# Optimization experiments

Measured on AMD Instinct MI355X. Metric: run time of the kernel, lower is better.

## Reference

```python
import jax, jax.numpy as jnp
import numpy as np

DIM = 1024
NUM_HEADS = 16
HEAD_DIM = DIM // NUM_HEADS


def apply_rotary_embed(x, thetas):
    # x: (..., seq, d), thetas: (seq, d) broadcast over leading dims
    x1, x2 = jnp.split(x, 2, axis=-1)
    x_rot = jnp.concatenate([-x2, x1], axis=-1)
    return x * jnp.cos(thetas) + x_rot * jnp.sin(thetas)


def setup_inputs() -> dict:
    key = jax.random.key(0)
    ks = jax.random.split(key, 8)
    B, Nx, Nc = 4, 1024, 2048
    x = jax.random.normal(ks[0], (B, Nx, DIM), dtype=jnp.float32)
    c = jax.random.normal(ks[1], (B, Nc, DIM), dtype=jnp.float32)
    x_pos_embed = jax.random.normal(ks[2], (Nx, HEAD_DIM), dtype=jnp.float32)
    c_pos_embed = jax.random.normal(ks[3], (Nc, HEAD_DIM), dtype=jnp.float32)
    s = 1.0 / np.sqrt(DIM)
    Wq = jax.random.normal(ks[4], (DIM, DIM), dtype=jnp.float32) * s
    Wkv = jax.random.normal(ks[5], (DIM, 2 * DIM), dtype=jnp.float32) * s
    Wproj = jax.random.normal(ks[6], (DIM, DIM), dtype=jnp.float32) * s
    bproj = jnp.zeros((DIM,), dtype=jnp.float32)
    return {"x": x, "c": c, "x_pos_embed": x_pos_embed, "c_pos_embed": c_pos_embed,
            "Wq": Wq, "Wkv": Wkv, "Wproj": Wproj, "bproj": bproj}


def reference(x, c, x_pos_embed, c_pos_embed, Wq, Wkv, Wproj, bproj):
    B, Nx, D = x.shape
    Nc = c.shape[1]
    H, hd = NUM_HEADS, HEAD_DIM
    # Q projection -> (B, H, Nx, hd)
    q = (x @ Wq).reshape(B, Nx, H, hd).transpose(0, 2, 1, 3)
    q = apply_rotary_embed(q, x_pos_embed)
    # KV projection -> k, v each (B, H, Nc, hd)
    kv = (c @ Wkv).reshape(B, Nc, 2, H, hd).transpose(2, 0, 3, 1, 4)
    k, v = kv[0], kv[1]
    k = apply_rotary_embed(k, c_pos_embed)
    # scaled dot-product attention (dropout p=0 -> identity)
    scale = 1.0 / np.sqrt(hd).astype(np.float32)
    attn = jnp.einsum('bhqd,bhkd->bhqk', q, k) * scale
    attn = jax.nn.softmax(attn, axis=-1)
    out = jnp.einsum('bhqk,bhkd->bhqd', attn, v)
    out = out.transpose(0, 2, 1, 3).reshape(B, Nx, D)
    return out @ Wproj + bproj
```

## Files before the change

kernel.cpp:

```cpp
#include <hip/hip_runtime.h>
#include <math.h>

#define DIMC  1024
#define NHEAD 16
#define HD    64
#define NB    4
#define NX    1024
#define NC    2048
#define KD    1024

typedef _Float16 half_t;
typedef __attribute__((ext_vector_type(8))) _Float16 h8;
typedef __attribute__((ext_vector_type(4))) _Float16 h4;
typedef __attribute__((ext_vector_type(2))) __fp16 fp16x2;
typedef __attribute__((ext_vector_type(4))) float f32x4;

#define QSCALE 0.1803368801111244f
#define NEGM  -8.656170245333781f

__device__ __forceinline__ void gload_lds16(const half_t* g, half_t* l) {
    __builtin_amdgcn_global_load_lds(
        (__attribute__((address_space(1))) void*)(g),
        (__attribute__((address_space(3))) void*)(l), 16, 0, 0);
}

__device__ __forceinline__ void wtile(const float* __restrict__ W,
                                      half_t* __restrict__ Wt, int N, int IMG,
                                      int bx, int by, int t)
{
    __shared__ half_t T[64][72];
    const int k0 = by * 64, n0 = bx * 64;
    const int kr = t >> 2, c0 = (t & 3) << 4;
    const float* src = W + (size_t)(k0 + kr) * N + n0 + c0;
#pragma unroll
    for (int j = 0; j < 16; j += 4) {
        float4 v = *(const float4*)(src + j);
        T[c0 + j + 0][kr] = (half_t)v.x;
        T[c0 + j + 1][kr] = (half_t)v.y;
        T[c0 + j + 2][kr] = (half_t)v.z;
        T[c0 + j + 3][kr] = (half_t)v.w;
    }
    __syncthreads();
    const int nr = t >> 2, kc = (t & 3) << 4;
    if (!IMG) {
        half_t* dst = Wt + (size_t)(n0 + nr) * KD + k0 + kc;
        *(int4*)dst       = *(const int4*)&T[nr][kc];
        *(int4*)(dst + 8) = *(const int4*)&T[nr][kc + 8];
    } else {
        const int n = n0 + nr;
        const int ntile = n >> 8, rr = n & 255;
        const int s0 = kc >> 3;
        half_t* base = Wt + ((size_t)(ntile * 16 + by) * 256 + rr) * 64;
        *(int4*)(base + ((s0 ^ (rr & 7)) << 3))       = *(const int4*)&T[nr][kc];
        *(int4*)(base + (((s0 + 1) ^ (rr & 7)) << 3)) = *(const int4*)&T[nr][kc + 8];
    }
}

__global__ __launch_bounds__(256) void prep(
    const float* __restrict__ x, half_t* __restrict__ xh,
    const float* __restrict__ c, half_t* __restrict__ ch,
    const float* __restrict__ xpe, const float* __restrict__ cpe,
    float* __restrict__ xct, float* __restrict__ xst,
    float* __restrict__ cct, float* __restrict__ cst,
    const float* __restrict__ Wq,  half_t* __restrict__ Wqt,
    const float* __restrict__ Wkv, half_t* __restrict__ Wkt,
    const float* __restrict__ Wp,  half_t* __restrict__ Wpt)
{
    const int bid = blockIdx.x, t = threadIdx.x;
    if (bid < 1024) {
        if (bid < 256)      wtile(Wq,  Wqt, DIMC, 1,     bid & 15,         bid >> 4,         t);
        else if (bid < 768) wtile(Wkv, Wkt, 2 * DIMC, 1, (bid - 256) & 31, (bid - 256) >> 5, t);
        else                wtile(Wp,  Wpt, DIMC, 0,     (bid - 768) & 15, (bid - 768) >> 4, t);
    } else if (bid < 7168) {
        const int nx = NB * NX * DIMC;
        const int i = ((bid - 1024) * 256 + t) * 8;
        h8 o;
        if (i < nx) {
            const float* s = x + i;
            float4 a = *(const float4*)(s);
            float4 b = *(const float4*)(s + 4);
            o[0] = (half_t)a.x; o[1] = (half_t)a.y; o[2] = (half_t)a.z; o[3] = (half_t)a.w;
            o[4] = (half_t)b.x; o[5] = (half_t)b.y; o[6] = (half_t)b.z; o[7] = (half_t)b.w;
            const int R = i >> 10, k = i & 1023;
            const int mt = R >> 8, r = R & 255, kt = k >> 6, sl = (k & 63) >> 3;
            *(h8*)(xh + ((size_t)(mt * 16 + kt) * 256 + r) * 64 + ((sl ^ (r & 7)) << 3)) = o;
        } else {
            const int j = i - nx;
            const float* s = c + j;
            float4 a = *(const float4*)(s);
            float4 b = *(const float4*)(s + 4);
            o[0] = (half_t)a.x; o[1] = (half_t)a.y; o[2] = (half_t)a.z; o[3] = (half_t)a.w;
            o[4] = (half_t)b.x; o[5] = (half_t)b.y; o[6] = (half_t)b.z; o[7] = (half_t)b.w;
            const int R = j >> 10, k = j & 1023;
            const int mt = R >> 8, r = R & 255, kt = k >> 6, sl = (k & 63) >> 3;
            *(h8*)(ch + ((size_t)(mt * 16 + kt) * 256 + r) * 64 + ((sl ^ (r & 7)) << 3)) = o;
        }
    } else {
        const int i = (bid - 7168) * 256 + t;
        if (i < NX * HD) {
            const float th = xpe[i];
            xct[i] = cosf(th); xst[i] = sinf(th);
        } else {
            const int j = i - NX * HD;
            const float th = cpe[j];
            cct[j] = cosf(th); cst[j] = sinf(th);
        }
    }
}

template <int MODE, int BN>
__global__ __launch_bounds__(256) void hgemm(
    const half_t* __restrict__ Ag, const half_t* __restrict__ Bt,
    const float* __restrict__ ct, const float* __restrict__ st,
    const float* __restrict__ bias,
    void* __restrict__ out0, void* __restrict__ out1)
{
    constexpr int MI = (BN == 128) ? 4 : 2;
    constexpr int BLOADS = BN / 32;
    __shared__ half_t As[2][8192];
    __shared__ half_t Bs[2][BN * 64];

    const int tid = threadIdx.x;
    const int w = tid >> 6, lane = tid & 63;
    const int lr = lane & 15, lg = lane >> 4;
    const int wrOff = (BN == 128) ? (w >> 1) * 64 : w * 32;
    const int wcOff = (BN == 128) ? (w & 1) * 64 : 0;

    int lin = (int)blockIdx.x;
    lin = (lin & 7) * ((int)gridDim.x >> 3) + (lin >> 3);
    const int m0 = (lin >> 4) * 128, n0 = (lin & 15) * BN;

    f32x4 acc[MI][4];
#pragma unroll
    for (int i = 0; i < MI; ++i)
#pragma unroll
        for (int j = 0; j < 4; ++j) acc[i][j] = f32x4{0.f, 0.f, 0.f, 0.f};

    size_t gA[4], gB[BLOADS];
    int loff[4];
#pragma unroll
    for (int c = 0; c < 4; ++c) {
        const int L = c * 4096 + w * 1024 + lane * 16;
        const int row = L >> 7;
        const int ss = ((L >> 4) & 7) ^ (row & 7);
        gA[c] = (size_t)(m0 + row) * KD + ss * 8;
        if (c < BLOADS) gB[c] = (size_t)(n0 + row) * KD + ss * 8;
        loff[c] = c * 2048 + w * 512;
    }

#define HSTAGE(buf, kk) do {                                               \
        _Pragma("unroll")                                                  \
        for (int c = 0; c < 4; ++c) {                                      \
            gload_lds16(Ag + gA[c] + (kk) * 64, &As[buf][loff[c]]);        \
            if (c < BLOADS) gload_lds16(Bt + gB[c] + (kk) * 64, &Bs[buf][loff[c]]); \
        }                                                                  \
    } while (0)

    HSTAGE(0, 0);
    asm volatile("s_waitcnt vmcnt(0)" ::: "memory");
    __builtin_amdgcn_s_barrier();
    __builtin_amdgcn_sched_barrier(0);

    for (int k = 0; k < KD / 64; ++k) {
        const int cb = k & 1;
        if (k + 1 < KD / 64) {
            HSTAGE(cb ^ 1, k + 1);
            if constexpr (BLOADS == 4)
                asm volatile("s_waitcnt vmcnt(8)" ::: "memory");
            else
                asm volatile("s_waitcnt vmcnt(6)" ::: "memory");
        } else {
            asm volatile("s_waitcnt vmcnt(0)" ::: "memory");
        }
        __builtin_amdgcn_s_barrier();
        __builtin_amdgcn_sched_barrier(0);

        __builtin_amdgcn_s_setprio(1);
#pragma unroll
        for (int kc = 0; kc < 2; ++kc) {
            h8 af[MI], bf[4];
#pragma unroll
            for (int mi = 0; mi < MI; ++mi) {
                const int r = wrOff + mi * 16 + lr;
                af[mi] = *(const h8*)&As[cb][r * 64 + (((kc * 4 + lg) ^ (r & 7)) << 3)];
            }
#pragma unroll
            for (int ni = 0; ni < 4; ++ni) {
                const int r = wcOff + ni * 16 + lr;
                bf[ni] = *(const h8*)&Bs[cb][r * 64 + (((kc * 4 + lg) ^ (r & 7)) << 3)];
            }
#pragma unroll
            for (int mi = 0; mi < MI; ++mi)
#pragma unroll
                for (int ni = 0; ni < 4; ++ni)
                    acc[mi][ni] = __builtin_amdgcn_mfma_f32_16x16x32_f16(
                        af[mi], bf[ni], acc[mi][ni], 0, 0, 0);
        }
        __builtin_amdgcn_s_setprio(0);

        __builtin_amdgcn_s_barrier();
        __builtin_amdgcn_sched_barrier(0);
    }
#undef HSTAGE

    if (MODE == 2) {
        float* o = (float*)out0;
#pragma unroll
        for (int ni = 0; ni < 4; ++ni) {
            const int col = n0 + ni * 16 + lr;
            const float bv = bias[col];
#pragma unroll
            for (int mi = 0; mi < MI; ++mi)
#pragma unroll
                for (int r = 0; r < 4; ++r) {
                    const int row = m0 + wrOff + mi * 16 + lg * 4 + r;
                    o[(size_t)row * DIMC + col] = acc[mi][ni][r] + bv;
                }
        }
    }
}

__global__ __launch_bounds__(512, 2) void hgemm_all(
    const half_t* __restrict__ Aimg, const half_t* __restrict__ Bimg,
    const half_t* __restrict__ Aq,   const half_t* __restrict__ Bq,
    const float* __restrict__ cct, const float* __restrict__ cst,
    const float* __restrict__ xct, const float* __restrict__ xst,
    half_t* __restrict__ Kw, half_t* __restrict__ Vw, half_t* __restrict__ Qw)
{
    __shared__ half_t lds[65536];

    const int tid = threadIdx.x;
    const int w = tid >> 6, lane = tid & 63;
    const int lr = lane & 15, lg = lane >> 4;
    const int wr = w >> 2, wc = w & 3;
    const int wrOff = wr * 128, wcOff = wc * 64;

    const int bid = (int)blockIdx.x;
    const bool isQ = bid >= 256;
    int m0, n0;
    const half_t* Ablk;
    const half_t* Bblk;
    if (!isQ) {
        int lin = (bid & 7) * 32 + (bid >> 3);
        const int mt = lin >> 3, nt = lin & 7;
        m0 = mt * 256; n0 = nt * 256;
        Ablk = Aimg + (size_t)mt * 262144;
        Bblk = Bimg + (size_t)nt * 262144;
    } else {
        const int q = bid - 256;
        int lin = (q & 7) * 8 + (q >> 3);
        const int mt = lin >> 2, nt = lin & 3;
        m0 = mt * 256; n0 = nt * 256;
        Ablk = Aq + (size_t)mt * 262144;
        Bblk = Bq + (size_t)nt * 262144;
    }
    const int so2 = w * 512 + lane * 8;

    f32x4 acc[8][4];
#pragma unroll
    for (int i = 0; i < 8; ++i)
#pragma unroll
        for (int j = 0; j < 4; ++j) acc[i][j] = f32x4{0.f, 0.f, 0.f, 0.f};
    h8 af[2][2];
    h8 bf[4][2];

#define ISSUEH(SRC, DSTOFF) do {                                     \
        gload_lds16((SRC) + so2,        &lds[(DSTOFF) + w * 512]);   \
        gload_lds16((SRC) + 4096 + so2, &lds[(DSTOFF) + 4096 + w * 512]); \
    } while (0)

#define PHASE(MI0, AOFF, BOFF, READBF, STG, GATE) do {               \
        _Pragma("unroll")                                            \
        for (int kc = 0; kc < 2; ++kc)                               \
        _Pragma("unroll")                                            \
        for (int d = 0; d < 2; ++d) {                                \
            const int r_ = wrOff + ((MI0) + d) * 16 + lr;            \
            af[d][kc] = *(const h8*)&lds[(AOFF) + r_ * 64 + (((kc * 4 + lg) ^ (r_ & 7)) << 3)]; \
        }                                                            \
        if (READBF) {                                                \
            _Pragma("unroll")                                        \
            for (int ni = 0; ni < 4; ++ni)                           \
            _Pragma("unroll")                                        \
            for (int kc = 0; kc < 2; ++kc) {                         \
                const int rb = wcOff + ni * 16 + lr;                 \
                bf[ni][kc] = *(const h8*)&lds[(BOFF) + rb * 64 + (((kc * 4 + lg) ^ (rb & 7)) << 3)]; \
            }                                                        \
        }                                                            \
        STG;                                                         \
        __builtin_amdgcn_sched_barrier(0);                           \
        __builtin_amdgcn_s_barrier();                                \
        __builtin_amdgcn_s_setprio(1);                               \
        _Pragma("unroll")                                            \
        for (int d = 0; d < 2; ++d)                                  \
        _Pragma("unroll")                                            \
        for (int ni = 0; ni < 4; ++ni)                               \
        _Pragma("unroll")                                            \
        for (int kc = 0; kc < 2; ++kc)                               \
            acc[(MI0) + d][ni] = __builtin_amdgcn_mfma_f32_16x16x32_f16( \
                af[d][kc], bf[ni][kc], acc[(MI0) + d][ni], 0, 0, 0); \
        __builtin_amdgcn_s_setprio(0);                               \
        GATE;                                                        \
        __builtin_amdgcn_s_barrier();                                \
    } while (0)

#define GATE4 asm volatile("s_waitcnt vmcnt(4)" ::: "memory")
#define GATE0 asm volatile("s_waitcnt vmcnt(0)" ::: "memory")
#define NOG   ((void)0)

    ISSUEH(Ablk, 0);          ISSUEH(Ablk + 8192, 8192);
    ISSUEH(Bblk, 32768);      ISSUEH(Bblk + 8192, 32768 + 8192);
    __builtin_amdgcn_sched_barrier(0);
    ISSUEH(Bblk + 16384, 49152); ISSUEH(Bblk + 16384 + 8192, 49152 + 8192);
    asm volatile("s_waitcnt vmcnt(4)" ::: "memory");
    __builtin_amdgcn_s_barrier();

    for (int i = 0; i < 7; ++i) {
        const half_t* An1 = Ablk + (size_t)(2 * i + 1) * 16384;
        const half_t* An2 = Ablk + (size_t)(2 * i + 2) * 16384;
        const half_t* Bn2 = Bblk + (size_t)(2 * i + 2) * 16384;
        const half_t* Bn3 = Bblk + (size_t)(2 * i + 3) * 16384;
        PHASE(0, 0,     32768, true,  ISSUEH(An1, 16384),               NOG);
        PHASE(2, 0,     32768, false, ISSUEH(An1 + 8192, 16384 + 8192), NOG);
        PHASE(4, 0,     32768, false, ISSUEH(Bn2, 32768),               NOG);
        PHASE(6, 0,     32768, false, ISSUEH(Bn2 + 8192, 32768 + 8192), GATE4);
        PHASE(0, 16384, 49152, true,  ISSUEH(An2, 0),                   NOG);
        PHASE(2, 16384, 49152, false, ISSUEH(An2 + 8192, 8192),         NOG);
        PHASE(4, 16384, 49152, false, ISSUEH(Bn3, 49152),               NOG);
        PHASE(6, 16384, 49152, false, ISSUEH(Bn3 + 8192, 49152 + 8192), GATE4);
    }
    {
        const half_t* A15 = Ablk + (size_t)15 * 16384;
        PHASE(0, 0,     32768, true,  ISSUEH(A15, 16384),               NOG);
        PHASE(2, 0,     32768, false, ISSUEH(A15 + 8192, 16384 + 8192), NOG);
        PHASE(4, 0,     32768, false, NOG,                              NOG);
        PHASE(6, 0,     32768, false, NOG,                              GATE0);
        PHASE(0, 16384, 49152, true,  NOG,                              NOG);
        PHASE(2, 16384, 49152, false, NOG,                              NOG);
        PHASE(4, 16384, 49152, false, NOG,                              NOG);
        PHASE(6, 16384, 49152, false, NOG,                              NOG);
    }
#undef PHASE
#undef ISSUEH
#undef GATE4
#undef GATE0
#undef NOG

    if (!isQ) {
        const bool isK = (n0 < DIMC);
        const int h = ((n0 & (DIMC - 1)) >> 6) + wc;
#pragma unroll
        for (int mi = 0; mi < 8; ++mi)
#pragma unroll
            for (int r = 0; r < 4; ++r) {
                const int row = m0 + wrOff + mi * 16 + lg * 4 + r;
                const int bb = row >> 11, nn = row & (NC - 1);
                const int tt = nn >> 6, rr = nn & 63;
                const size_t tbase = ((size_t)(bb * NHEAD + h) * 32 + tt) * 4096;
                const float* cr = cct + nn * HD;
                const float* sr = cst + nn * HD;
#pragma unroll
                for (int ni = 0; ni < 4; ++ni) {
                    const int d = ni * 16 + lr;
                    const float val = acc[mi][ni][r];
                    if (isK) {
                        const float pv = acc[mi][ni ^ 2][r];
                        Kw[tbase + rr * 64 + ((((d >> 3) ^ (rr & 7)) << 3) | (d & 7))] =
                            (half_t)(val * cr[d] + (ni < 2 ? -pv : pv) * sr[d]);
                    } else {
                        Vw[tbase + d * 64 + ((((rr >> 3) ^ (d & 7)) << 3) | (rr & 7))] =
                            (half_t)val;
                    }
                }
            }
    } else {
        const int h = (n0 >> 6) + wc;
#pragma unroll
        for (int mi = 0; mi < 8; ++mi)
#pragma unroll
            for (int r = 0; r < 4; ++r) {
                const int row = m0 + wrOff + mi * 16 + lg * 4 + r;
                const int bb = row >> 10, nn = row & (NX - 1);
                const float* cr = xct + nn * HD;
                const float* sr = xst + nn * HD;
                half_t* op = Qw + (((size_t)(bb * NHEAD + h)) * NX + nn) * HD;
#pragma unroll
                for (int ni = 0; ni < 4; ++ni) {
                    const int d = ni * 16 + lr;
                    const float val = acc[mi][ni][r];
                    const float pv  = acc[mi][ni ^ 2][r];
                    op[d] = (half_t)((val * cr[d] + (ni < 2 ? -pv : pv) * sr[d]) * QSCALE);
                }
            }
    }
}

__global__ __launch_bounds__(256) void attn_mfma(
    const half_t* __restrict__ Q, const half_t* __restrict__ Kg,
    const half_t* __restrict__ Vg,
    float* __restrict__ Opart, float* __restrict__ Lpart)
{
    __shared__ half_t Ks[3][4096];
    __shared__ half_t Vs[3][4096];
    __shared__ half_t Ps[16384];

    const int tid = threadIdx.x;
    const int w = tid >> 6, lane = tid & 63;
    const int lr = lane & 15, lg = lane >> 4;
    const int e7 = lr & 7;

    const int inner = (int)blockIdx.x & 255;
    const int kvh = (int)blockIdx.x >> 8;
    const int sid = (inner & 7) * 32 + (inner >> 3);
    const int bh = sid >> 2;
    const int q0 = (sid & 3) * 256;

    h8 qf0[4], qf1[4];
#pragma unroll
    for (int qb = 0; qb < 4; ++qb) {
        const half_t* qbase =
            Q + ((size_t)bh * NX + q0 + qb * 64 + w * 16 + lr) * HD + lg * 8;
        qf0[qb] = *(const h8*)(qbase);
        qf1[qb] = *(const h8*)(qbase + 32);
    }

    f32x4 acc[4][4];
#pragma unroll
    for (int qb = 0; qb < 4; ++qb)
#pragma unroll
        for (int i = 0; i < 4; ++i) acc[qb][i] = f32x4{0.f, 0.f, 0.f, 0.f};
    f32x4 accl[4];
#pragma unroll
    for (int qb = 0; qb < 4; ++qb) accl[qb] = f32x4{0.f, 0.f, 0.f, 0.f};

    h8 vone;
#pragma unroll
    for (int i = 0; i < 8; ++i) vone[i] = (half_t)(lr == 0 ? 1.0f : 0.0f);

    const half_t* Kt = Kg + (size_t)bh * 32 * 4096;
    const half_t* Vt = Vg + (size_t)bh * 32 * 4096;
    const int so = w * 512 + lane * 8;
    const int t0 = kvh * 16;

#define STAGE(bi, t) do {                                           \
        const half_t* kg_ = Kt + (size_t)(t) * 4096;                \
        const half_t* vg_ = Vt + (size_t)(t) * 4096;                \
        gload_lds16(kg_ + so,        &Ks[bi][w * 512]);             \
        gload_lds16(kg_ + 2048 + so, &Ks[bi][2048 + w * 512]);      \
        gload_lds16(vg_ + so,        &Vs[bi][w * 512]);             \
        gload_lds16(vg_ + 2048 + so, &Vs[bi][2048 + w * 512]);      \
    } while (0)

    STAGE(0, t0);

    const int rowq = w * 16 + lr;

    int cur = 0, nxt = 1;
    for (int i = 0; i < 16; ++i) {
        if (i + 1 < 16) {
            STAGE(nxt, t0 + i + 1);
            asm volatile("s_waitcnt vmcnt(4)" ::: "memory");
        } else {
            asm volatile("s_waitcnt vmcnt(0)" ::: "memory");
        }
        __builtin_amdgcn_s_barrier();
        __builtin_amdgcn_sched_barrier(0);

        h8 kfr[4][2];
#pragma unroll
        for (int cb = 0; cb < 4; ++cb) {
            const int r = cb * 16 + lr;
            kfr[cb][0] = *(const h8*)&Ks[cur][r * 64 + ((lg ^ e7) << 3)];
            kfr[cb][1] = *(const h8*)&Ks[cur][r * 64 + (((4 + lg) ^ e7) << 3)];
        }

#pragma unroll
        for (int qb = 0; qb < 4; ++qb) {
            const int rowp = qb * 64 + rowq;

            f32x4 sc[4];
            __builtin_amdgcn_s_setprio(1);
#pragma unroll
            for (int cb = 0; cb < 4; ++cb) {
                f32x4 a = {NEGM, NEGM, NEGM, NEGM};
                a = __builtin_amdgcn_mfma_f32_16x16x32_f16(kfr[cb][0], qf0[qb], a, 0, 0, 0);
                a = __builtin_amdgcn_mfma_f32_16x16x32_f16(kfr[cb][1], qf1[qb], a, 0, 0, 0);
                sc[cb] = a;
            }
            __builtin_amdgcn_s_setprio(0);

#pragma unroll
            for (int cb = 0; cb < 4; ++cb) {
                fp16x2 a01 = __builtin_amdgcn_cvt_pkrtz(exp2f(sc[cb][0]), exp2f(sc[cb][1]));
                fp16x2 a23 = __builtin_amdgcn_cvt_pkrtz(exp2f(sc[cb][2]), exp2f(sc[cb][3]));
                union { h4 h; uint2 u; } pw;
                pw.u.x = *(unsigned int*)&a01;
                pw.u.y = *(unsigned int*)&a23;
                const int s = cb * 2 + (lg >> 1);
                *(h4*)&Ps[rowp * 64 + ((s ^ e7) << 3) + (lg & 1) * 4] = pw.h;
            }
        }

        h8 pf0q[4], pf1q[4];
#pragma unroll
        for (int qb = 0; qb < 4; ++qb) {
            const int rowp = qb * 64 + rowq;
            pf0q[qb] = *(const h8*)&Ps[rowp * 64 + ((lg ^ e7) << 3)];
            pf1q[qb] = *(const h8*)&Ps[rowp * 64 + (((4 + lg) ^ e7) << 3)];
        }

        __builtin_amdgcn_s_setprio(1);
#pragma unroll
        for (int db = 0; db < 4; ++db) {
            const int rd = db * 16 + lr;
            const h8 vf0 = *(const h8*)&Vs[cur][rd * 64 + ((lg ^ e7) << 3)];
            const h8 vf1 = *(const h8*)&Vs[cur][rd * 64 + (((4 + lg) ^ e7) << 3)];
#pragma unroll
            for (int qb = 0; qb < 4; ++qb) {
                acc[qb][db] = __builtin_amdgcn_mfma_f32_16x16x32_f16(pf0q[qb], vf0, acc[qb][db], 0, 0, 0);
                acc[qb][db] = __builtin_amdgcn_mfma_f32_16x16x32_f16(pf1q[qb], vf1, acc[qb][db], 0, 0, 0);
            }
        }
#pragma unroll
        for (int qb = 0; qb < 4; ++qb) {
            accl[qb] = __builtin_amdgcn_mfma_f32_16x16x32_f16(pf0q[qb], vone, accl[qb], 0, 0, 0);
            accl[qb] = __builtin_amdgcn_mfma_f32_16x16x32_f16(pf1q[qb], vone, accl[qb], 0, 0, 0);
        }
        __builtin_amdgcn_s_setprio(0);

        cur = nxt;
        nxt = (nxt == 2) ? 0 : nxt + 1;
    }
#undef STAGE

#pragma unroll
    for (int qb = 0; qb < 4; ++qb) {
        const int qblk = (q0 >> 6) + qb;
        const int slot = (bh * 16 + qblk) * 2 + kvh;
        float* Po = Opart + (size_t)slot * 4096;
#pragma unroll
        for (int db = 0; db < 4; ++db)
#pragma unroll
            for (int r = 0; r < 4; ++r)
                Po[(w * 16 + lg * 4 + r) * 64 + db * 16 + lr] = acc[qb][db][r];
        if (lr == 0) {
#pragma unroll
            for (int r = 0; r < 4; ++r)
                Lpart[(size_t)slot * 64 + w * 16 + lg * 4 + r] = accl[qb][r];
        }
    }
}

__global__ __launch_bounds__(256) void combine(
    const float* __restrict__ Opart, const float* __restrict__ Lpart,
    half_t* __restrict__ Ow)
{
    const int pidx = blockIdx.x;
    const int bh = pidx >> 4, qblk = pidx & 15;
    const int b = bh >> 4, h = bh & 15;
    const int t = threadIdx.x;
    const int row = t >> 2;
    const int c0 = (t & 3) << 4;

    const float* P0 = Opart + (size_t)(pidx * 2 + 0) * 4096 + row * 64 + c0;
    const float* P1 = Opart + (size_t)(pidx * 2 + 1) * 4096 + row * 64 + c0;
    const float inv = 1.f / (Lpart[(size_t)(pidx * 2 + 0) * 64 + row] +
                             Lpart[(size_t)(pidx * 2 + 1) * 64 + row]);

    half_t* o = Ow + ((size_t)b * NX + qblk * 64 + row) * DIMC + h * 64 + c0;
#pragma unroll
    for (int j = 0; j < 16; j += 8) {
        float4 a0 = *(const float4*)(P0 + j);
        float4 a1 = *(const float4*)(P0 + j + 4);
        float4 b0 = *(const float4*)(P1 + j);
        float4 b1 = *(const float4*)(P1 + j + 4);
        h8 ov;
        ov[0] = (half_t)((a0.x + b0.x) * inv);
        ov[1] = (half_t)((a0.y + b0.y) * inv);
        ov[2] = (half_t)((a0.z + b0.z) * inv);
        ov[3] = (half_t)((a0.w + b0.w) * inv);
        ov[4] = (half_t)((a1.x + b1.x) * inv);
        ov[5] = (half_t)((a1.y + b1.y) * inv);
        ov[6] = (half_t)((a1.z + b1.z) * inv);
        ov[7] = (half_t)((a1.w + b1.w) * inv);
        *(h8*)(o + j) = ov;
    }
}

extern "C" void kernel_launch(void* const* d_in, const int* in_sizes, int n_in,
                              void* d_out, int out_size, void* d_ws, size_t ws_size,
                              hipStream_t stream)
{
    const float* x     = (const float*)d_in[0];
    const float* c     = (const float*)d_in[1];
    const float* xpe   = (const float*)d_in[2];
    const float* cpe   = (const float*)d_in[3];
    const float* Wq    = (const float*)d_in[4];
    const float* Wkv   = (const float*)d_in[5];
    const float* Wproj = (const float*)d_in[6];
    const float* bproj = (const float*)d_in[7];

    char* wsb = (char*)d_ws;
    half_t* xh  = (half_t*)(wsb);
    half_t* ch  = (half_t*)(wsb + ((size_t)8  << 20));
    half_t* Wqt = (half_t*)(wsb + ((size_t)24 << 20));
    half_t* Wkt = (half_t*)(wsb + ((size_t)26 << 20));
    half_t* Kw  = (half_t*)(wsb + ((size_t)32 << 20));
    half_t* Vw  = (half_t*)(wsb + ((size_t)48 << 20));
    half_t* Ow  = (half_t*)(wsb + ((size_t)64 << 20));
    float*  xct = (float*)(wsb + ((size_t)72 << 20));
    float*  xst = (float*)(wsb + ((size_t)72 << 20) + (256u << 10));
    float*  cct = (float*)(wsb + ((size_t)72 << 20) + (512u << 10));
    float*  cst = (float*)(wsb + ((size_t)72 << 20) + (1024u << 10));
    half_t* Wpt = (half_t*)(wsb + ((size_t)74 << 20));
    float*  Lpart = (float*)(wsb + ((size_t)76 << 20));
    float*  Opart = (float*)(wsb);
    half_t* Qw  = (half_t*)d_out;

    prep<<<7936, 256, 0, stream>>>(x, xh, c, ch, xpe, cpe,
                                   xct, xst, cct, cst,
                                   Wq, Wqt, Wkv, Wkt, Wproj, Wpt);

    hgemm_all<<<320, 512, 0, stream>>>(ch, Wkt, xh, Wqt,
                                       cct, cst, xct, xst,
                                       Kw, Vw, Qw);
    attn_mfma<<<512, 256, 0, stream>>>(Qw, Kw, Vw, Opart, Lpart);
    combine<<<1024, 256, 0, stream>>>(Opart, Lpart, Ow);
    hgemm<2, 64><<<512, 256, 0, stream>>>(Ow, Wpt, nullptr, nullptr, bproj,
                                          (float*)d_out, nullptr);
}
```

Before: 175.1 us.

## Shrink fused QKV GEMM tile to 256x128 and double grid for occupancy

Result: no change. 172.2 us, median of 2 (-1.6%).

```diff
diff --git a/kernel.cpp b/kernel.cpp
--- a/kernel.cpp
+++ b/kernel.cpp
@@ -220,48 +220,48 @@
     }
 }
 
-__global__ __launch_bounds__(512, 2) void hgemm_all(
+__global__ __launch_bounds__(512, 4) void hgemm_all(
     const half_t* __restrict__ Aimg, const half_t* __restrict__ Bimg,
     const half_t* __restrict__ Aq,   const half_t* __restrict__ Bq,
     const float* __restrict__ cct, const float* __restrict__ cst,
     const float* __restrict__ xct, const float* __restrict__ xst,
     half_t* __restrict__ Kw, half_t* __restrict__ Vw, half_t* __restrict__ Qw)
 {
-    __shared__ half_t lds[65536];
+    __shared__ half_t lds[40960];
 
     const int tid = threadIdx.x;
     const int w = tid >> 6, lane = tid & 63;
     const int lr = lane & 15, lg = lane >> 4;
-    const int wr = w >> 2, wc = w & 3;
-    const int wrOff = wr * 128, wcOff = wc * 64;
+    const int wr = w >> 1, wc = w & 1;
+    const int wrOff = wr * 64, wcOff = wc * 64;
 
     const int bid = (int)blockIdx.x;
-    const bool isQ = bid >= 256;
+    const bool isQ = bid >= 512;
     int m0, n0;
     const half_t* Ablk;
     const half_t* Bblk;
     if (!isQ) {
-        int lin = (bid & 7) * 32 + (bid >> 3);
+        int lin = (bid & 7) * 64 + (bid >> 3);
+        const int mt = lin >> 4, nt = lin & 15;
+        m0 = mt * 256; n0 = nt * 128;
+        Ablk = Aimg + (size_t)mt * 262144;
+        Bblk = Bimg + (size_t)(nt >> 1) * 262144 + (size_t)(nt & 1) * 8192;
+    } else {
+        const int q = bid - 512;
+        int lin = (q & 7) * 16 + (q >> 3);
         const int mt = lin >> 3, nt = lin & 7;
-        m0 = mt * 256; n0 = nt * 256;
-        Ablk = Aimg + (size_t)mt * 262144;
-        Bblk = Bimg + (size_t)nt * 262144;
-    } else {
-        const int q = bid - 256;
-        int lin = (q & 7) * 8 + (q >> 3);
-        const int mt = lin >> 2, nt = lin & 3;
-        m0 = mt * 256; n0 = nt * 256;
+        m0 = mt * 256; n0 = nt * 128;
         Ablk = Aq + (size_t)mt * 262144;
-        Bblk = Bq + (size_t)nt * 262144;
+        Bblk = Bq + (size_t)(nt >> 1) * 262144 + (size_t)(nt & 1) * 8192;
     }
     const int so2 = w * 512 + lane * 8;
 
-    f32x4 acc[8][4];
-#pragma unroll
-    for (int i = 0; i < 8; ++i)
+    f32x4 acc[4][4];
+#pragma unroll
+    for (int i = 0; i < 4; ++i)
 #pragma unroll
         for (int j = 0; j < 4; ++j) acc[i][j] = f32x4{0.f, 0.f, 0.f, 0.f};
-    h8 af[2][2];
+    h8 af[2];
     h8 bf[4][2];
 
 #define ISSUEH(SRC, DSTOFF) do {                                     \
@@ -269,13 +269,12 @@
         gload_lds16((SRC) + 4096 + so2, &lds[(DSTOFF) + 4096 + w * 512]); \
     } while (0)
 
-#define PHASE(MI0, AOFF, BOFF, READBF, STG, GATE) do {               \
-        _Pragma("unroll")                                            \
-        for (int kc = 0; kc < 2; ++kc)                               \
-        _Pragma("unroll")                                            \
-        for (int d = 0; d < 2; ++d) {                                \
-            const int r_ = wrOff + ((MI0) + d) * 16 + lr;            \
-            af[d][kc] = *(const h8*)&lds[(AOFF) + r_ * 64 + (((kc * 4 + lg) ^ (r_ & 7)) << 3)]; \
+#define PHASE(MI0, AOFF, READBF, STG, GATE) do {                     \
+        {                                                            \
+            const int r_ = wrOff + (MI0) * 16 + lr;                  \
+            _Pragma("unroll")                                        \
+            for (int kc = 0; kc < 2; ++kc)                           \
+                af[kc] = *(const h8*)&lds[(AOFF) + r_ * 64 + (((kc * 4 + lg) ^ (r_ & 7)) << 3)]; \
         }                                                            \
         if (READBF) {                                                \
             _Pragma("unroll")                                        \
@@ -283,7 +282,7 @@
             _Pragma("unroll")                                        \
             for (int kc = 0; kc < 2; ++kc) {                         \
                 const int rb = wcOff + ni * 16 + lr;                 \
-                bf[ni][kc] = *(const h8*)&lds[(BOFF) + rb * 64 + (((kc * 4 + lg) ^ (rb & 7)) << 3)]; \
+                bf[ni][kc] = *(const h8*)&lds[32768 + rb * 64 + (((kc * 4 + lg) ^ (rb & 7)) << 3)]; \
             }                                                        \
         }                                                            \
         STG;                                                         \
@@ -291,57 +290,40 @@
         __builtin_amdgcn_s_barrier();                                \
         __builtin_amdgcn_s_setprio(1);                               \
         _Pragma("unroll")                                            \
-        for (int d = 0; d < 2; ++d)                                  \
-        _Pragma("unroll")                                            \
         for (int ni = 0; ni < 4; ++ni)                               \
         _Pragma("unroll")                                            \
         for (int kc = 0; kc < 2; ++kc)                               \
-            acc[(MI0) + d][ni] = __builtin_amdgcn_mfma_f32_16x16x32_f16( \
-                af[d][kc], bf[ni][kc], acc[(MI0) + d][ni], 0, 0, 0); \
+            acc[(MI0)][ni] = __builtin_amdgcn_mfma_f32_16x16x32_f16( \
+                af[kc], bf[ni][kc], acc[(MI0)][ni], 0, 0, 0);        \
         __builtin_amdgcn_s_setprio(0);                               \
         GATE;                                                        \
         __builtin_amdgcn_s_barrier();                                \
     } while (0)
 
-#define GATE4 asm volatile("s_waitcnt vmcnt(4)" ::: "memory")
 #define GATE0 asm volatile("s_waitcnt vmcnt(0)" ::: "memory")
 #define NOG   ((void)0)
 
-    ISSUEH(Ablk, 0);          ISSUEH(Ablk + 8192, 8192);
-    ISSUEH(Bblk, 32768);      ISSUEH(Bblk + 8192, 32768 + 8192);
+    ISSUEH(Ablk, 0);
+    ISSUEH(Ablk + 8192, 8192);
+    ISSUEH(Bblk, 32768);
+    asm volatile("s_waitcnt vmcnt(0)" ::: "memory");
+    __builtin_amdgcn_s_barrier();
     __builtin_amdgcn_sched_barrier(0);
-    ISSUEH(Bblk + 16384, 49152); ISSUEH(Bblk + 16384 + 8192, 49152 + 8192);
-    asm volatile("s_waitcnt vmcnt(4)" ::: "memory");
-    __builtin_amdgcn_s_barrier();
-
-    for (int i = 0; i < 7; ++i) {
-        const half_t* An1 = Ablk + (size_t)(2 * i + 1) * 16384;
-        const half_t* An2 = Ablk + (size_t)(2 * i + 2) * 16384;
-        const half_t* Bn2 = Bblk + (size_t)(2 * i + 2) * 16384;
-        const half_t* Bn3 = Bblk + (size_t)(2 * i + 3) * 16384;
-        PHASE(0, 0,     32768, true,  ISSUEH(An1, 16384),               NOG);
-        PHASE(2, 0,     32768, false, ISSUEH(An1 + 8192, 16384 + 8192), NOG);
-        PHASE(4, 0,     32768, false, ISSUEH(Bn2, 32768),               NOG);
-        PHASE(6, 0,     32768, false, ISSUEH(Bn2 + 8192, 32768 + 8192), GATE4);
-        PHASE(0, 16384, 49152, true,  ISSUEH(An2, 0),                   NOG);
-        PHASE(2, 16384, 49152, false, ISSUEH(An2 + 8192, 8192),         NOG);
-        PHASE(4, 16384, 49152, false, ISSUEH(Bn3, 49152),               NOG);
-        PHASE(6, 16384, 49152, false, ISSUEH(Bn3 + 8192, 49152 + 8192), GATE4);
-    }
-    {
-        const half_t* A15 = Ablk + (size_t)15 * 16384;
-        PHASE(0, 0,     32768, true,  ISSUEH(A15, 16384),               NOG);
-        PHASE(2, 0,     32768, false, ISSUEH(A15 + 8192, 16384 + 8192), NOG);
-        PHASE(4, 0,     32768, false, NOG,                              NOG);
-        PHASE(6, 0,     32768, false, NOG,                              GATE0);
-        PHASE(0, 16384, 49152, true,  NOG,                              NOG);
-        PHASE(2, 16384, 49152, false, NOG,                              NOG);
-        PHASE(4, 16384, 49152, false, NOG,                              NOG);
-        PHASE(6, 16384, 49152, false, NOG,                              NOG);
+
+#pragma unroll 2
+    for (int t = 0; t < 16; ++t) {
+        const int AOFF = (t & 1) ? 16384 : 0;
+        const int ALT  = (t & 1) ? 0 : 16384;
+        const half_t* An = Ablk + (size_t)(t + 1) * 16384;
+        const half_t* Bn = Bblk + (size_t)(t + 1) * 16384;
+        const bool more = (t + 1 < 16);
+        PHASE(0, AOFF, true,  NOG,                                        NOG);
+        PHASE(1, AOFF, false, if (more) ISSUEH(Bn, 32768),                NOG);
+        PHASE(2, AOFF, false, if (more) ISSUEH(An, ALT),                  NOG);
+        PHASE(3, AOFF, false, if (more) ISSUEH(An + 8192, ALT + 8192),    GATE0);
     }
 #undef PHASE
 #undef ISSUEH
-#undef GATE4
 #undef GATE0
 #undef NOG
 
@@ -349,7 +331,7 @@
         const bool isK = (n0 < DIMC);
         const int h = ((n0 & (DIMC - 1)) >> 6) + wc;
 #pragma unroll
-        for (int mi = 0; mi < 8; ++mi)
+        for (int mi = 0; mi < 4; ++mi)
 #pragma unroll
             for (int r = 0; r < 4; ++r) {
                 const int row = m0 + wrOff + mi * 16 + lg * 4 + r;
@@ -375,7 +357,7 @@
     } else {
         const int h = (n0 >> 6) + wc;
 #pragma unroll
-        for (int mi = 0; mi < 8; ++mi)
+        for (int mi = 0; mi < 4; ++mi)
 #pragma unroll
             for (int r = 0; r < 4; ++r) {
                 const int row = m0 + wrOff + mi * 16 + lg * 4 + r;
@@ -620,7 +602,7 @@
                                    xct, xst, cct, cst,
                                    Wq, Wqt, Wkv, Wkt, Wproj, Wpt);
 
-    hgemm_all<<<320, 512, 0, stream>>>(ch, Wkt, xh, Wqt,
+    hgemm_all<<<640, 512, 0, stream>>>(ch, Wkt, xh, Wqt,
                                        cct, cst, xct, xst,
                                        Kw, Vw, Qw);
     attn_mfma<<<512, 256, 0, stream>>>(Qw, Kw, Vw, Opart, Lpart);
```
